# Performance work log

Hardware: AMD Instinct MI355X
Metric: run time of the kernel (lower is better)

The kernel has to match this reference:

```python
import jax, jax.numpy as jnp
import numpy as np

TEMPERATURE = 8.0  # sqrt(d_k), d_k = 64
B, L, D = 32, 2048, 64


def setup_inputs() -> dict:
    key = jax.random.key(0)
    kq, kk, kv, kd, km = jax.random.split(key, 5)
    q = jax.random.normal(kq, (B, L, D), dtype=jnp.float32)
    k = jax.random.normal(kk, (B, L, D), dtype=jnp.float32)
    v = jax.random.normal(kv, (B, L, D), dtype=jnp.float32)
    diag_mask = jax.random.randint(kd, (B, L, L), 0, 2, dtype=jnp.int32)
    mask = jax.random.randint(km, (B, L, L), 0, 2).astype(jnp.bool_)
    return {"q": q, "k": k, "v": v, "diag_mask": diag_mask, "mask": mask}


def reference(q, k, v, diag_mask, mask):
    # attn = (q @ k^T) / temperature              [B, L, L]
    attn = jnp.einsum("bqd,bkd->bqk", q, k) / TEMPERATURE
    # optional mask: masked_fill(mask, -inf)
    attn = jnp.where(mask, -jnp.inf, attn)
    # diag mask: masked_fill(diag_mask == 0, -1e32)
    attn = jnp.where(diag_mask == 0, jnp.float32(-1e32), attn)
    attn = jax.nn.softmax(attn, axis=-1)
    # output = attn @ v                            [B, L, D]
    output = jnp.einsum("bqk,bkd->bqd", attn, v)
    return (output, attn)
```

## Files before the change

kernel.cpp:

```cpp
#include <hip/hip_runtime.h>
#include <cstdint>
#include <cstddef>

#define BB 32
#define LL 2048
#define DD 64

#define BIG_NEG (-3.0e38f)

__global__ __launch_bounds__(256) void k_scores(
    const float* __restrict__ q, const float* __restrict__ kmat,
    const int* __restrict__ diag, const int* __restrict__ mask,
    float* __restrict__ attn)
{
    __shared__ __align__(16) float sQT[32][132];
    __shared__ __align__(16) float sKT[32][132];

    const int b  = blockIdx.z;
    const int q0 = blockIdx.y * 128;
    const int k0 = blockIdx.x * 128;
    const int t  = threadIdx.x;
    const int tx = t & 15;
    const int ty = t >> 4;

    const float* qb = q    + ((size_t)b * LL + q0) * DD;
    const float* kb = kmat + ((size_t)b * LL + k0) * DD;

    float acc[8][8];
    #pragma unroll
    for (int i = 0; i < 8; ++i)
        #pragma unroll
        for (int j = 0; j < 8; ++j) acc[i][j] = 0.0f;

    for (int dc = 0; dc < DD; dc += 32) {
        #pragma unroll
        for (int i = 0; i < 4; ++i) {
            int lin = t + 256 * i;
            int row = lin >> 3;
            int dv  = lin & 7;
            float4 a = *(const float4*)(qb + (size_t)row * DD + dc + dv * 4);
            sQT[dv * 4 + 0][row] = a.x;
            sQT[dv * 4 + 1][row] = a.y;
            sQT[dv * 4 + 2][row] = a.z;
            sQT[dv * 4 + 3][row] = a.w;
            float4 c = *(const float4*)(kb + (size_t)row * DD + dc + dv * 4);
            sKT[dv * 4 + 0][row] = c.x;
            sKT[dv * 4 + 1][row] = c.y;
            sKT[dv * 4 + 2][row] = c.z;
            sKT[dv * 4 + 3][row] = c.w;
        }
        __syncthreads();

        #pragma unroll 8
        for (int d = 0; d < 32; ++d) {
            float4 a0 = *(const float4*)&sQT[d][ty * 8];
            float4 a1 = *(const float4*)&sQT[d][ty * 8 + 4];
            float4 b0 = *(const float4*)&sKT[d][tx * 8];
            float4 b1 = *(const float4*)&sKT[d][tx * 8 + 4];
            float aa[8] = {a0.x, a0.y, a0.z, a0.w, a1.x, a1.y, a1.z, a1.w};
            float bb[8] = {b0.x, b0.y, b0.z, b0.w, b1.x, b1.y, b1.z, b1.w};
            #pragma unroll
            for (int ri = 0; ri < 8; ++ri)
                #pragma unroll
                for (int ci = 0; ci < 8; ++ci)
                    acc[ri][ci] = fmaf(aa[ri], bb[ci], acc[ri][ci]);
        }
        __syncthreads();
    }

    #pragma unroll
    for (int ri = 0; ri < 8; ++ri) {
        int qq = q0 + ty * 8 + ri;
        size_t base = ((size_t)b * LL + qq) * LL + (size_t)(k0 + tx * 8);
        int4 dm0 = *(const int4*)(diag + base);
        int4 dm1 = *(const int4*)(diag + base + 4);
        int4 mk0 = *(const int4*)(mask + base);
        int4 mk1 = *(const int4*)(mask + base + 4);
        int dmv[8] = {dm0.x, dm0.y, dm0.z, dm0.w, dm1.x, dm1.y, dm1.z, dm1.w};
        int mkv[8] = {mk0.x, mk0.y, mk0.z, mk0.w, mk1.x, mk1.y, mk1.z, mk1.w};
        float o[8];
        #pragma unroll
        for (int ci = 0; ci < 8; ++ci) {
            float s = acc[ri][ci] * 0.125f;
            o[ci] = (dmv[ci] == 0 || mkv[ci] != 0) ? BIG_NEG : s;
        }
        *(float4*)(attn + base)     = make_float4(o[0], o[1], o[2], o[3]);
        *(float4*)(attn + base + 4) = make_float4(o[4], o[5], o[6], o[7]);
    }
}

__global__ __launch_bounds__(256) void k_softmax(float* __restrict__ attn)
{
    __shared__ float redm[4];
    __shared__ float reds[4];
    float* p = attn + (size_t)blockIdx.x * LL;
    const int t = threadIdx.x;
    const int wave = t >> 6, lane = t & 63;

    float4 x0 = ((const float4*)p)[t];
    float4 x1 = ((const float4*)p)[t + 256];

    float m = fmaxf(fmaxf(fmaxf(x0.x, x0.y), fmaxf(x0.z, x0.w)),
                    fmaxf(fmaxf(x1.x, x1.y), fmaxf(x1.z, x1.w)));
    #pragma unroll
    for (int off = 32; off >= 1; off >>= 1)
        m = fmaxf(m, __shfl_xor(m, off, 64));
    if (lane == 0) redm[wave] = m;
    __syncthreads();
    m = fmaxf(fmaxf(redm[0], redm[1]), fmaxf(redm[2], redm[3]));

    x0.x = expf(x0.x - m); x0.y = expf(x0.y - m);
    x0.z = expf(x0.z - m); x0.w = expf(x0.w - m);
    x1.x = expf(x1.x - m); x1.y = expf(x1.y - m);
    x1.z = expf(x1.z - m); x1.w = expf(x1.w - m);

    float s = (x0.x + x0.y + x0.z + x0.w) + (x1.x + x1.y + x1.z + x1.w);
    #pragma unroll
    for (int off = 32; off >= 1; off >>= 1)
        s += __shfl_xor(s, off, 64);
    if (lane == 0) reds[wave] = s;
    __syncthreads();
    s = (reds[0] + reds[1]) + (reds[2] + reds[3]);

    float inv = 1.0f / s;
    x0.x *= inv; x0.y *= inv; x0.z *= inv; x0.w *= inv;
    x1.x *= inv; x1.y *= inv; x1.z *= inv; x1.w *= inv;
    ((float4*)p)[t]       = x0;
    ((float4*)p)[t + 256] = x1;
}

__global__ __launch_bounds__(256) void k_pv(
    const float* __restrict__ attn, const float* __restrict__ v,
    float* __restrict__ out)
{
    __shared__ __align__(16) float sPT[64][132];
    __shared__ __align__(16) float sV[64][68];

    const int b  = blockIdx.y;
    const int q0 = blockIdx.x * 128;
    const int t  = threadIdx.x;
    const int tx = t & 15;
    const int ty = t >> 4;

    const float* pb = attn + ((size_t)b * LL + q0) * LL;
    const float* vb = v + (size_t)b * LL * DD;

    float acc[8][4];
    #pragma unroll
    for (int i = 0; i < 8; ++i)
        #pragma unroll
        for (int j = 0; j < 4; ++j) acc[i][j] = 0.0f;

    for (int k0 = 0; k0 < LL; k0 += 64) {
        #pragma unroll
        for (int i = 0; i < 8; ++i) {
            int lin = t + 256 * i;
            int row = lin >> 4;
            int kv  = lin & 15;
            float4 a = *(const float4*)(pb + (size_t)row * LL + k0 + kv * 4);
            sPT[kv * 4 + 0][row] = a.x;
            sPT[kv * 4 + 1][row] = a.y;
            sPT[kv * 4 + 2][row] = a.z;
            sPT[kv * 4 + 3][row] = a.w;
        }
        #pragma unroll
        for (int i = 0; i < 4; ++i) {
            int lin = t + 256 * i;
            int row = lin >> 4;
            int dv  = lin & 15;
            *(float4*)&sV[row][dv * 4] =
                *(const float4*)(vb + (size_t)(k0 + row) * DD + dv * 4);
        }
        __syncthreads();

        #pragma unroll 8
        for (int kk = 0; kk < 64; ++kk) {
            float4 a0 = *(const float4*)&sPT[kk][ty * 8];
            float4 a1 = *(const float4*)&sPT[kk][ty * 8 + 4];
            float4 b0 = *(const float4*)&sV[kk][tx * 4];
            float aa[8] = {a0.x, a0.y, a0.z, a0.w, a1.x, a1.y, a1.z, a1.w};
            float bb[4] = {b0.x, b0.y, b0.z, b0.w};
            #pragma unroll
            for (int ri = 0; ri < 8; ++ri)
                #pragma unroll
                for (int ci = 0; ci < 4; ++ci)
                    acc[ri][ci] = fmaf(aa[ri], bb[ci], acc[ri][ci]);
        }
        __syncthreads();
    }

    #pragma unroll
    for (int ri = 0; ri < 8; ++ri) {
        float4 o = make_float4(acc[ri][0], acc[ri][1], acc[ri][2], acc[ri][3]);
        *(float4*)(out + ((size_t)b * LL + q0 + ty * 8 + ri) * DD + tx * 4) = o;
    }
}

extern "C" void kernel_launch(void* const* d_in, const int* in_sizes, int n_in,
                              void* d_out, int out_size, void* d_ws, size_t ws_size,
                              hipStream_t stream)
{
    const float* q    = (const float*)d_in[0];
    const float* k    = (const float*)d_in[1];
    const float* v    = (const float*)d_in[2];
    const int*   diag = (const int*)d_in[3];
    const int*   mask = (const int*)d_in[4];

    float* out  = (float*)d_out;
    float* attn = out + (size_t)BB * LL * DD;

    k_scores <<<dim3(LL / 128, LL / 128, BB), 256, 0, stream>>>(q, k, diag, mask, attn);
    k_softmax<<<dim3(BB * LL),                256, 0, stream>>>(attn);
    k_pv     <<<dim3(LL / 128, BB),           256, 0, stream>>>(attn, v, out);
}
```

Measured before the change: 1.684 ms.

## Fuse softmax normalization into PV kernel using per-tile partial row statistics

The scores kernel now emits per-tile row max and exp-sum partials. A small reduce kernel combines these into a per-row max and inverse sum. The PV kernel then applies exp and normalization while loading attention tiles, writes the normalized probabilities back, and uses them for the matmul. This removes the separate softmax pass's full read of the attention matrix, at the cost of extra work and stores in the low-occupancy PV kernel. Shared-memory tiles are also padded and rotated, with the column mapping changed, to reduce bank conflicts.

```diff
diff --git a/kernel.cpp b/kernel.cpp
--- a/kernel.cpp
+++ b/kernel.cpp
@@ -5,16 +5,17 @@
 #define BB 32
 #define LL 2048
 #define DD 64
+#define NKB 16
 
 #define BIG_NEG (-3.0e38f)
 
 __global__ __launch_bounds__(256) void k_scores(
     const float* __restrict__ q, const float* __restrict__ kmat,
     const int* __restrict__ diag, const int* __restrict__ mask,
-    float* __restrict__ attn)
-{
-    __shared__ __align__(16) float sQT[32][132];
-    __shared__ __align__(16) float sKT[32][132];
+    float* __restrict__ attn, float* __restrict__ pm, float* __restrict__ pl)
+{
+    __shared__ __align__(16) float sQT[32][156];
+    __shared__ __align__(16) float sKT[32][156];
 
     const int b  = blockIdx.z;
     const int q0 = blockIdx.y * 128;
@@ -22,6 +23,8 @@
     const int t  = threadIdx.x;
     const int tx = t & 15;
     const int ty = t >> 4;
+    const int tyb = ty * 8;
+    const int txb = tx * 4;
 
     const float* qb = q    + ((size_t)b * LL + q0) * DD;
     const float* kb = kmat + ((size_t)b * LL + k0) * DD;
@@ -38,25 +41,27 @@
             int lin = t + 256 * i;
             int row = lin >> 3;
             int dv  = lin & 7;
+            int cc  = row + dv * 4;
             float4 a = *(const float4*)(qb + (size_t)row * DD + dc + dv * 4);
-            sQT[dv * 4 + 0][row] = a.x;
-            sQT[dv * 4 + 1][row] = a.y;
-            sQT[dv * 4 + 2][row] = a.z;
-            sQT[dv * 4 + 3][row] = a.w;
-            float4 c = *(const float4*)(kb + (size_t)row * DD + dc + dv * 4);
-            sKT[dv * 4 + 0][row] = c.x;
-            sKT[dv * 4 + 1][row] = c.y;
-            sKT[dv * 4 + 2][row] = c.z;
-            sKT[dv * 4 + 3][row] = c.w;
+            sQT[dv * 4 + 0][cc] = a.x;
+            sQT[dv * 4 + 1][cc] = a.y;
+            sQT[dv * 4 + 2][cc] = a.z;
+            sQT[dv * 4 + 3][cc] = a.w;
+            float4 c4 = *(const float4*)(kb + (size_t)row * DD + dc + dv * 4);
+            sKT[dv * 4 + 0][cc] = c4.x;
+            sKT[dv * 4 + 1][cc] = c4.y;
+            sKT[dv * 4 + 2][cc] = c4.z;
+            sKT[dv * 4 + 3][cc] = c4.w;
         }
         __syncthreads();
 
-        #pragma unroll 8
+        #pragma unroll
         for (int d = 0; d < 32; ++d) {
-            float4 a0 = *(const float4*)&sQT[d][ty * 8];
-            float4 a1 = *(const float4*)&sQT[d][ty * 8 + 4];
-            float4 b0 = *(const float4*)&sKT[d][tx * 8];
-            float4 b1 = *(const float4*)&sKT[d][tx * 8 + 4];
+            const int rot = d & 28;
+            float4 a0 = *(const float4*)&sQT[d][tyb + rot];
+            float4 a1 = *(const float4*)&sQT[d][tyb + 4 + rot];
+            float4 b0 = *(const float4*)&sKT[d][txb + rot];
+            float4 b1 = *(const float4*)&sKT[d][txb + 64 + rot];
             float aa[8] = {a0.x, a0.y, a0.z, a0.w, a1.x, a1.y, a1.z, a1.w};
             float bb[8] = {b0.x, b0.y, b0.z, b0.w, b1.x, b1.y, b1.z, b1.w};
             #pragma unroll
@@ -70,12 +75,14 @@
 
     #pragma unroll
     for (int ri = 0; ri < 8; ++ri) {
-        int qq = q0 + ty * 8 + ri;
-        size_t base = ((size_t)b * LL + qq) * LL + (size_t)(k0 + tx * 8);
-        int4 dm0 = *(const int4*)(diag + base);
-        int4 dm1 = *(const int4*)(diag + base + 4);
-        int4 mk0 = *(const int4*)(mask + base);
-        int4 mk1 = *(const int4*)(mask + base + 4);
+        int qq = q0 + tyb + ri;
+        size_t rb    = ((size_t)b * LL + qq) * LL + k0;
+        size_t base0 = rb + txb;
+        size_t base1 = rb + txb + 64;
+        int4 dm0 = *(const int4*)(diag + base0);
+        int4 dm1 = *(const int4*)(diag + base1);
+        int4 mk0 = *(const int4*)(mask + base0);
+        int4 mk1 = *(const int4*)(mask + base1);
         int dmv[8] = {dm0.x, dm0.y, dm0.z, dm0.w, dm1.x, dm1.y, dm1.z, dm1.w};
         int mkv[8] = {mk0.x, mk0.y, mk0.z, mk0.w, mk1.x, mk1.y, mk1.z, mk1.w};
         float o[8];
@@ -84,9 +91,87 @@
             float s = acc[ri][ci] * 0.125f;
             o[ci] = (dmv[ci] == 0 || mkv[ci] != 0) ? BIG_NEG : s;
         }
-        *(float4*)(attn + base)     = make_float4(o[0], o[1], o[2], o[3]);
-        *(float4*)(attn + base + 4) = make_float4(o[4], o[5], o[6], o[7]);
-    }
+        *(float4*)(attn + base0) = make_float4(o[0], o[1], o[2], o[3]);
+        *(float4*)(attn + base1) = make_float4(o[4], o[5], o[6], o[7]);
+
+        if (pm != nullptr) {
+            float rm = fmaxf(fmaxf(fmaxf(o[0], o[1]), fmaxf(o[2], o[3])),
+                             fmaxf(fmaxf(o[4], o[5]), fmaxf(o[6], o[7])));
+            #pragma unroll
+            for (int off = 8; off >= 1; off >>= 1)
+                rm = fmaxf(rm, __shfl_xor(rm, off, 64));
+            float rs = 0.0f;
+            #pragma unroll
+            for (int ci = 0; ci < 8; ++ci) rs += __expf(o[ci] - rm);
+            #pragma unroll
+            for (int off = 8; off >= 1; off >>= 1)
+                rs += __shfl_xor(rs, off, 64);
+            if (tx == 0) {
+                size_t pidx = ((size_t)b * LL + qq) * NKB + blockIdx.x;
+                pm[pidx] = rm;
+                pl[pidx] = rs;
+            }
+        }
+    }
+}
+
+__global__ __launch_bounds__(256) void k_reduce(
+    const float* __restrict__ pm, const float* __restrict__ pl,
+    float2* __restrict__ stats)
+{
+    int row = blockIdx.x * 256 + threadIdx.x;
+    const float4* m4 = (const float4*)(pm + (size_t)row * NKB);
+    const float4* l4 = (const float4*)(pl + (size_t)row * NKB);
+    float4 m0 = m4[0], m1 = m4[1], m2 = m4[2], m3 = m4[3];
+    float4 l0 = l4[0], l1 = l4[1], l2 = l4[2], l3 = l4[3];
+    float m = fmaxf(fmaxf(fmaxf(fmaxf(m0.x, m0.y), fmaxf(m0.z, m0.w)),
+                          fmaxf(fmaxf(m1.x, m1.y), fmaxf(m1.z, m1.w))),
+                    fmaxf(fmaxf(fmaxf(m2.x, m2.y), fmaxf(m2.z, m2.w)),
+                          fmaxf(fmaxf(m3.x, m3.y), fmaxf(m3.z, m3.w))));
+    float l = l0.x * __expf(m0.x - m) + l0.y * __expf(m0.y - m)
+            + l0.z * __expf(m0.z - m) + l0.w * __expf(m0.w - m)
+            + l1.x * __expf(m1.x - m) + l1.y * __expf(m1.y - m)
+            + l1.z * __expf(m1.z - m) + l1.w * __expf(m1.w - m)
+            + l2.x * __expf(m2.x - m) + l2.y * __expf(m2.y - m)
+            + l2.z * __expf(m2.z - m) + l2.w * __expf(m2.w - m)
+            + l3.x * __expf(m3.x - m) + l3.y * __expf(m3.y - m)
+            + l3.z * __expf(m3.z - m) + l3.w * __expf(m3.w - m);
+    stats[row] = make_float2(m, 1.0f / l);
+}
+
+__global__ __launch_bounds__(256) void k_rowstats(
+    const float* __restrict__ attn, float2* __restrict__ stats)
+{
+    __shared__ float redm[4];
+    __shared__ float reds[4];
+    const float* p = attn + (size_t)blockIdx.x * LL;
+    const int t = threadIdx.x;
+    const int wave = t >> 6, lane = t & 63;
+
+    float4 x0 = ((const float4*)p)[t];
+    float4 x1 = ((const float4*)p)[t + 256];
+
+    float m = fmaxf(fmaxf(fmaxf(x0.x, x0.y), fmaxf(x0.z, x0.w)),
+                    fmaxf(fmaxf(x1.x, x1.y), fmaxf(x1.z, x1.w)));
+    #pragma unroll
+    for (int off = 32; off >= 1; off >>= 1)
+        m = fmaxf(m, __shfl_xor(m, off, 64));
+    if (lane == 0) redm[wave] = m;
+    __syncthreads();
+    m = fmaxf(fmaxf(redm[0], redm[1]), fmaxf(redm[2], redm[3]));
+
+    float s = __expf(x0.x - m) + __expf(x0.y - m)
+            + __expf(x0.z - m) + __expf(x0.w - m)
+            + __expf(x1.x - m) + __expf(x1.y - m)
+            + __expf(x1.z - m) + __expf(x1.w - m);
+    #pragma unroll
+    for (int off = 32; off >= 1; off >>= 1)
+        s += __shfl_xor(s, off, 64);
+    if (lane == 0) reds[wave] = s;
+    __syncthreads();
+    s = (reds[0] + reds[1]) + (reds[2] + reds[3]);
+
+    if (t == 0) stats[blockIdx.x] = make_float2(m, 1.0f / s);
 }
 
 __global__ __launch_bounds__(256) void k_softmax(float* __restrict__ attn)
@@ -129,21 +214,32 @@
     ((float4*)p)[t + 256] = x1;
 }
 
-__global__ __launch_bounds__(256) void k_pv(
-    const float* __restrict__ attn, const float* __restrict__ v,
-    float* __restrict__ out)
-{
-    __shared__ __align__(16) float sPT[64][132];
+__global__ __launch_bounds__(256) void k_pv_softmax(
+    float* __restrict__ attn, const float* __restrict__ v,
+    const float2* __restrict__ stats, float* __restrict__ out)
+{
+    __shared__ __align__(16) float sPT[64][188];
     __shared__ __align__(16) float sV[64][68];
+    __shared__ float sM[128];
+    __shared__ float sIL[128];
 
     const int b  = blockIdx.y;
     const int q0 = blockIdx.x * 128;
     const int t  = threadIdx.x;
     const int tx = t & 15;
     const int ty = t >> 4;
-
-    const float* pb = attn + ((size_t)b * LL + q0) * LL;
+    const int tyb = ty * 8;
+    const int txb = tx * 4;
+
+    float* pb = attn + ((size_t)b * LL + q0) * LL;
     const float* vb = v + (size_t)b * LL * DD;
+
+    if (stats != nullptr && t < 128) {
+        float2 st = stats[(size_t)b * LL + q0 + t];
+        sM[t]  = st.x;
+        sIL[t] = st.y;
+    }
+    __syncthreads();
 
     float acc[8][4];
     #pragma unroll
@@ -157,11 +253,22 @@
             int lin = t + 256 * i;
             int row = lin >> 4;
             int kv  = lin & 15;
-            float4 a = *(const float4*)(pb + (size_t)row * LL + k0 + kv * 4);
-            sPT[kv * 4 + 0][row] = a.x;
-            sPT[kv * 4 + 1][row] = a.y;
-            sPT[kv * 4 + 2][row] = a.z;
-            sPT[kv * 4 + 3][row] = a.w;
+            float* src = pb + (size_t)row * LL + k0 + kv * 4;
+            float4 a = *(const float4*)src;
+            if (stats != nullptr) {
+                float m  = sM[row];
+                float il = sIL[row];
+                a.x = __expf(a.x - m) * il;
+                a.y = __expf(a.y - m) * il;
+                a.z = __expf(a.z - m) * il;
+                a.w = __expf(a.w - m) * il;
+                *(float4*)src = a;
+            }
+            int cc = row + kv * 4;
+            sPT[kv * 4 + 0][cc] = a.x;
+            sPT[kv * 4 + 1][cc] = a.y;
+            sPT[kv * 4 + 2][cc] = a.z;
+            sPT[kv * 4 + 3][cc] = a.w;
         }
         #pragma unroll
         for (int i = 0; i < 4; ++i) {
@@ -173,11 +280,12 @@
         }
         __syncthreads();
 
-        #pragma unroll 8
+        #pragma unroll
         for (int kk = 0; kk < 64; ++kk) {
-            float4 a0 = *(const float4*)&sPT[kk][ty * 8];
-            float4 a1 = *(const float4*)&sPT[kk][ty * 8 + 4];
-            float4 b0 = *(const float4*)&sV[kk][tx * 4];
+            const int rot = kk & 60;
+            float4 a0 = *(const float4*)&sPT[kk][tyb + rot];
+            float4 a1 = *(const float4*)&sPT[kk][tyb + 4 + rot];
+            float4 b0 = *(const float4*)&sV[kk][txb];
             float aa[8] = {a0.x, a0.y, a0.z, a0.w, a1.x, a1.y, a1.z, a1.w};
             float bb[4] = {b0.x, b0.y, b0.z, b0.w};
             #pragma unroll
@@ -192,7 +300,7 @@
     #pragma unroll
     for (int ri = 0; ri < 8; ++ri) {
         float4 o = make_float4(acc[ri][0], acc[ri][1], acc[ri][2], acc[ri][3]);
-        *(float4*)(out + ((size_t)b * LL + q0 + ty * 8 + ri) * DD + tx * 4) = o;
+        *(float4*)(out + ((size_t)b * LL + q0 + tyb + ri) * DD + txb) = o;
     }
 }
 
@@ -209,7 +317,29 @@
     float* out  = (float*)d_out;
     float* attn = out + (size_t)BB * LL * DD;
 
-    k_scores <<<dim3(LL / 128, LL / 128, BB), 256, 0, stream>>>(q, k, diag, mask, attn);
-    k_softmax<<<dim3(BB * LL),                256, 0, stream>>>(attn);
-    k_pv     <<<dim3(LL / 128, BB),           256, 0, stream>>>(attn, v, out);
-}
+    const size_t ROWS = (size_t)BB * LL;
+    const size_t PART_FLOATS = ROWS * NKB;
+    const size_t needA = PART_FLOATS * 4 * 2 + ROWS * 8;
+    const size_t needB = ROWS * 8;
+
+    if (d_ws != nullptr && ws_size >= needA) {
+        float*  pm    = (float*)d_ws;
+        float*  pl    = pm + PART_FLOATS;
+        float2* stats = (float2*)(pl + PART_FLOATS);
+        k_scores    <<<dim3(LL / 128, LL / 128, BB), 256, 0, stream>>>(
+                        q, k, diag, mask, attn, pm, pl);
+        k_reduce    <<<dim3((int)(ROWS / 256)),       256, 0, stream>>>(pm, pl, stats);
+        k_pv_softmax<<<dim3(LL / 128, BB),            256, 0, stream>>>(attn, v, stats, out);
+    } else if (d_ws != nullptr && ws_size >= needB) {
+        float2* stats = (float2*)d_ws;
+        k_scores    <<<dim3(LL / 128, LL / 128, BB), 256, 0, stream>>>(
+                        q, k, diag, mask, attn, nullptr, nullptr);
+        k_rowstats  <<<dim3(BB * LL),                 256, 0, stream>>>(attn, stats);
+        k_pv_softmax<<<dim3(LL / 128, BB),            256, 0, stream>>>(attn, v, stats, out);
+    } else {
+        k_scores    <<<dim3(LL / 128, LL / 128, BB), 256, 0, stream>>>(
+                        q, k, diag, mask, attn, nullptr, nullptr);
+        k_softmax   <<<dim3(BB * LL),                 256, 0, stream>>>(attn);
+        k_pv_softmax<<<dim3(LL / 128, BB),            256, 0, stream>>>(attn, v, nullptr, out);
+    }
+}
```

New measurement: 1.878 ms. +11.6%, slower.
